# Optimization experiments

Measured on AMD Instinct MI355X. Metric: run time of the kernel, lower is better.

Reference implementation:

```python
import jax, jax.numpy as jnp
import numpy as np

B, E, S, DIM, HID, H = 8, 512, 1024, 1024, 1024, 8  # S == DIM == HID by construction


def setup_inputs() -> dict:
    key = jax.random.key(0)
    ks = jax.random.split(key, 7)
    x = jax.random.normal(ks[0], (B, E, S), dtype=jnp.float32)
    # per-head projection Linear(dim, hidden_dim): weight [H, hidden, dim], bias [H, hidden]
    proj_w = jax.random.normal(ks[1], (H, HID, DIM), dtype=jnp.float32) / np.sqrt(DIM)
    proj_b = jax.random.normal(ks[2], (H, HID), dtype=jnp.float32) * 0.02
    # per-head ColRepeatCausalLinear: weight [H, S] (torch.randn(1, dim)), bias [H, S] (zeros init)
    mix_w = jax.random.normal(ks[3], (H, S), dtype=jnp.float32)
    mix_b = jnp.zeros((H, S), dtype=jnp.float32)
    # out_proj Linear(dim, dim)
    out_w = jax.random.normal(ks[4], (DIM, DIM), dtype=jnp.float32) / np.sqrt(DIM)
    out_b = jax.random.normal(ks[5], (DIM,), dtype=jnp.float32) * 0.02
    return {"x": x, "proj_w": proj_w, "proj_b": proj_b, "mix_w": mix_w,
            "mix_b": mix_b, "out_w": out_w, "out_b": out_b, "index": 0}


def reference(x, proj_w, proj_b, mix_w, mix_b, out_w, out_b, index):
    # Per-head linear projection on the last axis (grouped GEMM across heads).
    # proj: [B, H, E, HID]
    proj = jnp.einsum('bes,hds->bhed', x, proj_w) + proj_b[None, :, None, :]
    # ColRepeatCausalLinear parallel path with decay_value == 1:
    # W[i, j] = v[j] for j >= i  =>  (x @ W)[..., j] = v[j] * cumsum(x, -1)[..., j]
    mixed = mix_w[None, :, None, :] * jnp.cumsum(proj, axis=-1) + mix_b[None, :, None, :]
    # torch.cat(activations, dim=1): [B, H*E, S]
    hidden = mixed.reshape(B, H * E, S)
    # out_proj Linear(dim, dim) on last axis
    out = hidden @ out_w.T + out_b
    return out
```

## Files before the change

kernel.cpp:

```cpp
#include <hip/hip_runtime.h>

#define NH    8
#define NE    512
#define NB    8
#define ND    1024
#define NROW  4096

typedef unsigned short u16;
typedef __attribute__((ext_vector_type(8))) short short8;
typedef __attribute__((ext_vector_type(4))) float f32x4;

__device__ __forceinline__ u16 f2bf(float f) {
  unsigned int u = __float_as_uint(f);
  u += 0x7fffu + ((u >> 16) & 1u);
  return (u16)(u >> 16);
}

__device__ __forceinline__ void gload16(const u16* g, u16* l) {
  __builtin_amdgcn_global_load_lds(
      (const __attribute__((address_space(1))) unsigned int*)(const void*)g,
      (__attribute__((address_space(3))) unsigned int*)(void*)l, 16, 0, 0);
}

__global__ __launch_bounds__(256) void fused_pre_kernel(
    const float* __restrict__ X, u16* __restrict__ Xb,
    const float* __restrict__ W, u16* __restrict__ Wt,
    const float* __restrict__ out_w, const float* __restrict__ mix_w,
    const float* __restrict__ mix_b, const float* __restrict__ proj_b,
    const float* __restrict__ out_b,
    u16* __restrict__ Afac, float* __restrict__ Kc) {
  __shared__ float tile[64][65];
  __shared__ float wsum[4];
  __shared__ float red[4];
  const int bz = blockIdx.x;
  const int t  = threadIdx.x;

  if (bz < 1024) {
    const int o = bz;
    const int lane = t & 63, wave = t >> 6;
    float ow[4];
#pragma unroll
    for (int k = 0; k < 4; ++k) ow[k] = out_w[(size_t)o * ND + 1023 - (4 * t + k)];
    float ob = out_b[o];
#pragma unroll 1
    for (int h = 0; h < NH; ++h) {
      const float* mwr = mix_w + (size_t)h * ND;
      const float* mbr = mix_b + (size_t)h * ND;
      const float* pbr = proj_b + (size_t)h * ND;
      float l[4];
      float run = 0.f, mbdot = 0.f;
#pragma unroll
      for (int k = 0; k < 4; ++k) {
        int j = 1023 - (4 * t + k);
        mbdot += ow[k] * mbr[j];
        run += ow[k] * mwr[j];
        l[k] = run;
      }
      float tsum = run;
      float sc = tsum;
#pragma unroll
      for (int d = 1; d < 64; d <<= 1) {
        float other = __shfl_up(sc, d);
        if (lane >= d) sc += other;
      }
      if (lane == 63) wsum[wave] = sc;
      __syncthreads();
      float wprefix = 0.f;
      for (int w = 0; w < wave; ++w) wprefix += wsum[w];
      float excl = wprefix + sc - tsum;

      float cdot = 0.f;
      ushort4 pack;
      u16* pk = (u16*)&pack;
#pragma unroll
      for (int k = 0; k < 4; ++k) {
        int d = 1023 - (4 * t + k);
        float a = excl + l[k];
        cdot += a * pbr[d];
        pk[3 - k] = f2bf(a);
      }
      *(ushort4*)(Afac + ((size_t)(h * ND + o)) * ND + (1020 - 4 * t)) = pack;

      float tot = cdot + mbdot;
#pragma unroll
      for (int m = 32; m >= 1; m >>= 1) tot += __shfl_xor(tot, m);
      if (lane == 0) red[wave] = tot;
      __syncthreads();
      if (t == 0) Kc[h * ND + o] = red[0] + red[1] + red[2] + red[3] + ob;
    }
  } else if (bz < 3072) {
    const int f  = bz - 1024;
    const int h  = f >> 8;
    const int d0 = ((f >> 4) & 15) * 64;
    const int s0 = (f & 15) * 64;
    const int tr = t >> 4;
    const int tc = t & 15;
#pragma unroll
    for (int i = 0; i < 4; ++i) {
      int d = tr + i * 16;
      float4 v = *(const float4*)(W + ((size_t)h * ND + d0 + d) * ND + s0 + tc * 4);
      tile[d][tc * 4 + 0] = v.x;
      tile[d][tc * 4 + 1] = v.y;
      tile[d][tc * 4 + 2] = v.z;
      tile[d][tc * 4 + 3] = v.w;
    }
    __syncthreads();
#pragma unroll
    for (int i = 0; i < 4; ++i) {
      int s  = tr + i * 16;
      int dd = tc * 4;
      ushort4 o;
      o.x = f2bf(tile[dd + 0][s]);
      o.y = f2bf(tile[dd + 1][s]);
      o.z = f2bf(tile[dd + 2][s]);
      o.w = f2bf(tile[dd + 3][s]);
      *(ushort4*)(Wt + ((size_t)h * ND + s0 + s) * ND + d0 + dd) = o;
    }
  } else {
    int i = (bz - 3072) * 256 + t;
    float4 v = ((const float4*)X)[i];
    ushort4 o;
    o.x = f2bf(v.x); o.y = f2bf(v.y); o.z = f2bf(v.z); o.w = f2bf(v.w);
    ((ushort4*)Xb)[i] = o;
  }
}

#define MFMA_(d, a, b) d = __builtin_amdgcn_mfma_f32_16x16x32_bf16(a, b, d, 0, 0, 0)
#define NOVM ((void)0)
#define VM6 asm volatile("s_waitcnt vmcnt(6)" ::: "memory")
#define VM5 asm volatile("s_waitcnt vmcnt(5)" ::: "memory")
#define VM0 asm volatile("s_waitcnt vmcnt(0)" ::: "memory")

#define PHASE(q, b, STAGE_STMT, VMSTMT) do {                                   \
    short8 a00 = ldA(b, 2*(q),     0);                                         \
    short8 a01 = ldA(b, 2*(q),     1);                                         \
    short8 a10 = ldA(b, 2*(q) + 1, 0);                                         \
    short8 a11 = ldA(b, 2*(q) + 1, 1);                                         \
    if ((q) == 0) {                                                            \
      bf00 = ldB(b, 0, 0); bf01 = ldB(b, 0, 1);                                \
      bf10 = ldB(b, 1, 0); bf11 = ldB(b, 1, 1);                                \
      bf20 = ldB(b, 2, 0); bf21 = ldB(b, 2, 1);                                \
      bf30 = ldB(b, 3, 0); bf31 = ldB(b, 3, 1);                                \
    }                                                                          \
    STAGE_STMT;                                                                \
    __builtin_amdgcn_sched_barrier(0);                                         \
    VMSTMT;                                                                    \
    __builtin_amdgcn_s_barrier();                                              \
    asm volatile("s_waitcnt lgkmcnt(0)" ::: "memory");                         \
    __builtin_amdgcn_sched_barrier(0);                                         \
    __builtin_amdgcn_s_setprio(1);                                             \
    MFMA_(acc[2*(q)  ][0], a00, bf00);                                         \
    MFMA_(acc[2*(q)  ][1], a00, bf10);                                         \
    MFMA_(acc[2*(q)  ][2], a00, bf20);                                         \
    MFMA_(acc[2*(q)  ][3], a00, bf30);                                         \
    MFMA_(acc[2*(q)+1][0], a10, bf00);                                         \
    MFMA_(acc[2*(q)+1][1], a10, bf10);                                         \
    MFMA_(acc[2*(q)+1][2], a10, bf20);                                         \
    MFMA_(acc[2*(q)+1][3], a10, bf30);                                         \
    MFMA_(acc[2*(q)  ][0], a01, bf01);                                         \
    MFMA_(acc[2*(q)  ][1], a01, bf11);                                         \
    MFMA_(acc[2*(q)  ][2], a01, bf21);                                         \
    MFMA_(acc[2*(q)  ][3], a01, bf31);                                         \
    MFMA_(acc[2*(q)+1][0], a11, bf01);                                         \
    MFMA_(acc[2*(q)+1][1], a11, bf11);                                         \
    MFMA_(acc[2*(q)+1][2], a11, bf21);                                         \
    MFMA_(acc[2*(q)+1][3], a11, bf31);                                         \
    __builtin_amdgcn_s_setprio(0);                                             \
    __builtin_amdgcn_s_barrier();                                              \
  } while (0)

#define PHASE1(q, b, STAGE_STMT, VMSTMT) do {                                  \
    short8 a0 = ldA(b, (q), 0);                                                \
    short8 a1 = ldA(b, (q), 1);                                                \
    if ((q) == 0) {                                                            \
      bf00 = ldB(b, 0, 0); bf01 = ldB(b, 0, 1);                                \
      bf10 = ldB(b, 1, 0); bf11 = ldB(b, 1, 1);                                \
      bf20 = ldB(b, 2, 0); bf21 = ldB(b, 2, 1);                                \
      bf30 = ldB(b, 3, 0); bf31 = ldB(b, 3, 1);                                \
    }                                                                          \
    STAGE_STMT;                                                                \
    __builtin_amdgcn_sched_barrier(0);                                         \
    VMSTMT;                                                                    \
    __builtin_amdgcn_s_barrier();                                              \
    asm volatile("s_waitcnt lgkmcnt(0)" ::: "memory");                         \
    __builtin_amdgcn_sched_barrier(0);                                         \
    __builtin_amdgcn_s_setprio(1);                                             \
    MFMA_(acc[(q)][0], a0, bf00);                                              \
    MFMA_(acc[(q)][1], a0, bf10);                                              \
    MFMA_(acc[(q)][2], a0, bf20);                                              \
    MFMA_(acc[(q)][3], a0, bf30);                                              \
    MFMA_(acc[(q)][0], a1, bf01);                                              \
    MFMA_(acc[(q)][1], a1, bf11);                                              \
    MFMA_(acc[(q)][2], a1, bf21);                                              \
    MFMA_(acc[(q)][3], a1, bf31);                                              \
    __builtin_amdgcn_s_setprio(0);                                             \
    __builtin_amdgcn_s_barrier();                                              \
  } while (0)

#define GEMM_8PH_BODY(ASRC, BSRC)                                              \
  const int tid  = threadIdx.x;                                                \
  const int lane = tid & 63;                                                   \
  const int wave = tid >> 6;                                                   \
  const int wm   = wave >> 2;                                                  \
  const int wn   = wave & 3;                                                   \
  const int li8 = lane >> 3;                                                   \
  const int lc  = (lane & 7) ^ li8;                                            \
  const size_t stSrc = (size_t)li8 * ND + lc * 8;                              \
  const int stDst = lane * 8;                                                  \
  const u16* aSrc = (ASRC) + stSrc;                                            \
  const u16* bSrc = (BSRC) + stSrc;                                            \
  const int fr  = lane & 15;                                                   \
  const int rg  = lane >> 4;                                                   \
  const int ca0 = (((lane >> 4)    ) ^ (lane & 7)) * 8;                        \
  const int ca1 = (((lane >> 4) + 4) ^ (lane & 7)) * 8;                        \
  const int aOff = (wm * 128 + fr) * 64;                                       \
  const int bOff = 16384 + (wn * 64 + fr) * 64;                                \
  auto stageA = [&](int h, int t, int b) {                                     \
    _Pragma("unroll")                                                          \
    for (int jj = 0; jj < 2; ++jj) {                                           \
      int j = 2 * wave + jj;                                                   \
      int R = ((j >> 3) << 7) + h * 64 + ((j & 7) << 3);                       \
      gload16(aSrc + (size_t)R * ND + t * 64, lds + b * 32768 + R * 64 + stDst); \
    }                                                                          \
  };                                                                           \
  auto stageB = [&](int h, int t, int b) {                                     \
    _Pragma("unroll")                                                          \
    for (int jj = 0; jj < 2; ++jj) {                                           \
      int j = 2 * wave + jj;                                                   \
      int R = h * 128 + j * 8;                                                 \
      gload16(bSrc + (size_t)R * ND + t * 64, lds + b * 32768 + 16384 + R * 64 + stDst); \
    }                                                                          \
  };                                                                           \
  auto ldA = [&](int b, int mi, int kk) -> short8 {                            \
    return *(const short8*)(lds + b * 32768 + aOff + mi * 1024 + (kk ? ca1 : ca0)); \
  };                                                                           \
  auto ldB = [&](int b, int ni, int kk) -> short8 {                            \
    return *(const short8*)(lds + b * 32768 + bOff + ni * 1024 + (kk ? ca1 : ca0)); \
  };                                                                           \
  f32x4 acc[8][4];                                                             \
  f32x4 z = {0.f, 0.f, 0.f, 0.f};                                              \
  _Pragma("unroll")                                                            \
  for (int i = 0; i < 8; ++i)                                                  \
    _Pragma("unroll")                                                          \
    for (int j = 0; j < 4; ++j) acc[i][j] = z;                                 \
  short8 bf00, bf01, bf10, bf11, bf20, bf21, bf30, bf31;                       \
  stageA(0, 0, 0); stageA(1, 0, 0);                                            \
  stageB(0, 0, 0); stageB(1, 0, 0);                                            \
  stageB(0, 1, 1); stageB(1, 1, 1);                                            \
  stageA(0, 1, 1);                                                             \
  asm volatile("s_waitcnt vmcnt(6)" ::: "memory");                             \
  __builtin_amdgcn_s_barrier();                                                \
  _Pragma("unroll 1")                                                          \
  for (int it = 0; it < 7; ++it) {                                             \
    const int T = 2 * it;                                                      \
    PHASE(0, 0, stageA(1, T + 1, 1), NOVM);                                    \
    PHASE(1, 0, stageB(0, T + 2, 0), NOVM);                                    \
    PHASE(2, 0, stageB(1, T + 2, 0), NOVM);                                    \
    PHASE(3, 0, stageA(0, T + 2, 0), VM6);                                     \
    PHASE(0, 1, stageA(1, T + 2, 0), NOVM);                                    \
    PHASE(1, 1, stageB(0, T + 3, 1), NOVM);                                    \
    PHASE(2, 1, stageB(1, T + 3, 1), NOVM);                                    \
    PHASE(3, 1, stageA(0, T + 3, 1), VM6);                                     \
  }                                                                            \
  PHASE(0, 0, stageA(1, 15, 1), NOVM);                                         \
  PHASE(1, 0, NOVM, NOVM);                                                     \
  PHASE(2, 0, NOVM, NOVM);                                                     \
  PHASE(3, 0, NOVM, VM0);                                                      \
  PHASE(0, 1, NOVM, NOVM);                                                     \
  PHASE(1, 1, NOVM, NOVM);                                                     \
  PHASE(2, 1, NOVM, NOVM);                                                     \
  PHASE(3, 1, NOVM, NOVM);

__global__ __launch_bounds__(512, 2) void gemm1_8ph(const u16* __restrict__ Afac,
                                                    const u16* __restrict__ Wt,
                                                    u16* __restrict__ Mmat) {
  __shared__ __align__(16) u16 lds[49152];
  const int h  = blockIdx.z;
  const int m0 = blockIdx.y * 128;
  const int n0 = blockIdx.x * 256;
  const int tid  = threadIdx.x;
  const int lane = tid & 63;
  const int wave = tid >> 6;
  const int wm   = wave >> 2;
  const int wn   = wave & 3;
  const int li8 = lane >> 3;
  const int lc  = (lane & 7) ^ li8;
  const size_t stSrc = (size_t)li8 * ND + lc * 8;
  const int stDst = lane * 8;
  const u16* aSrc = Afac + ((size_t)h * ND + m0) * ND + stSrc;
  const u16* bSrc = Wt + ((size_t)h * ND + n0) * ND + stSrc;
  const int fr  = lane & 15;
  const int rg  = lane >> 4;
  const int ca0 = (((lane >> 4)    ) ^ (lane & 7)) * 8;
  const int ca1 = (((lane >> 4) + 4) ^ (lane & 7)) * 8;
  const int aOff = (wm * 64 + fr) * 64;
  const int bOff = 8192 + (wn * 64 + fr) * 64;

  auto stageA = [&](int h2, int t, int b) {
    int R = (wave >> 2) * 64 + h2 * 32 + (wave & 3) * 8;
    gload16(aSrc + (size_t)R * ND + t * 64, lds + b * 24576 + R * 64 + stDst);
  };
  auto stageB = [&](int h2, int t, int b) {
#pragma unroll
    for (int jj = 0; jj < 2; ++jj) {
      int j = 2 * wave + jj;
      int R = h2 * 128 + j * 8;
      gload16(bSrc + (size_t)R * ND + t * 64, lds + b * 24576 + 8192 + R * 64 + stDst);
    }
  };
  auto ldA = [&](int b, int mi, int kk) -> short8 {
    return *(const short8*)(lds + b * 24576 + aOff + mi * 1024 + (kk ? ca1 : ca0));
  };
  auto ldB = [&](int b, int ni, int kk) -> short8 {
    return *(const short8*)(lds + b * 24576 + bOff + ni * 1024 + (kk ? ca1 : ca0));
  };

  f32x4 acc[4][4];
  f32x4 z = {0.f, 0.f, 0.f, 0.f};
#pragma unroll
  for (int i = 0; i < 4; ++i)
#pragma unroll
    for (int j = 0; j < 4; ++j) acc[i][j] = z;
  short8 bf00, bf01, bf10, bf11, bf20, bf21, bf30, bf31;

  stageA(0, 0, 0); stageA(1, 0, 0);
  stageB(0, 0, 0); stageB(1, 0, 0);
  stageB(0, 1, 1); stageB(1, 1, 1);
  stageA(0, 1, 1);
  VM5;
  __builtin_amdgcn_s_barrier();

#pragma unroll 1
  for (int it = 0; it < 7; ++it) {
    const int T = 2 * it;
    PHASE1(0, 0, stageA(1, T + 1, 1), NOVM);
    PHASE1(1, 0, stageB(0, T + 2, 0), NOVM);
    PHASE1(2, 0, stageB(1, T + 2, 0), NOVM);
    PHASE1(3, 0, stageA(0, T + 2, 0), VM5);
    PHASE1(0, 1, stageA(1, T + 2, 0), NOVM);
    PHASE1(1, 1, stageB(0, T + 3, 1), NOVM);
    PHASE1(2, 1, stageB(1, T + 3, 1), NOVM);
    PHASE1(3, 1, stageA(0, T + 3, 1), VM5);
  }
  PHASE1(0, 0, stageA(1, 15, 1), NOVM);
  PHASE1(1, 0, NOVM, NOVM);
  PHASE1(2, 0, NOVM, NOVM);
  PHASE1(3, 0, NOVM, VM0);
  PHASE1(0, 1, NOVM, NOVM);
  PHASE1(1, 1, NOVM, NOVM);
  PHASE1(2, 1, NOVM, NOVM);
  PHASE1(3, 1, NOVM, NOVM);

  u16* Mh = Mmat + (size_t)h * ND * ND;
  const int r0 = m0 + wm * 64 + rg * 4;
  const int c0 = n0 + wn * 64 + fr;
#pragma unroll
  for (int mi = 0; mi < 4; ++mi) {
#pragma unroll
    for (int r = 0; r < 4; ++r) {
      u16* orow = Mh + (size_t)(r0 + mi * 16 + r) * ND + c0;
#pragma unroll
      for (int ni = 0; ni < 4; ++ni)
        orow[ni * 16] = f2bf(acc[mi][ni][r]);
    }
  }
}

__global__ __launch_bounds__(512, 2) void gemm2_8ph(const u16* __restrict__ Xb,
                                                    const u16* __restrict__ Bm,
                                                    const float* __restrict__ Kc,
                                                    float* __restrict__ Out) {
  __shared__ __align__(16) u16 lds[65536];
  const int bid = blockIdx.x;
  const int xcd = bid & 7;
  const int loc = bid >> 3;
  const int m0  = (((xcd >> 2) << 3) + (loc >> 3)) * 256;
  const int n0  = (((xcd & 3) << 3) + (loc & 7)) * 256;
  GEMM_8PH_BODY(Xb + (size_t)m0 * ND, Bm + (size_t)n0 * ND)

  const int hH = n0 >> 10;
  const int r0 = m0 + wm * 128 + rg * 4;
  const int c0 = n0 + wn * 64 + fr;
  const int o0 = c0 & 1023;
  float bias[4];
#pragma unroll
  for (int ni = 0; ni < 4; ++ni) bias[ni] = Kc[c0 + ni * 16];
#pragma unroll
  for (int mi = 0; mi < 8; ++mi) {
#pragma unroll
    for (int r = 0; r < 4; ++r) {
      int rb = r0 + mi * 16 + r;
      float* orow = Out + ((size_t)(rb >> 9) * 4096 + hH * 512 + (rb & 511)) * 1024 + o0;
#pragma unroll
      for (int ni = 0; ni < 4; ++ni)
        orow[ni * 16] = acc[mi][ni][r] + bias[ni];
    }
  }
}

extern "C" void kernel_launch(void* const* d_in, const int* in_sizes, int n_in,
                              void* d_out, int out_size, void* d_ws, size_t ws_size,
                              hipStream_t stream) {
  (void)in_sizes; (void)n_in; (void)out_size; (void)ws_size;
  const float* x      = (const float*)d_in[0];
  const float* proj_w = (const float*)d_in[1];
  const float* proj_b = (const float*)d_in[2];
  const float* mix_w  = (const float*)d_in[3];
  const float* mix_b  = (const float*)d_in[4];
  const float* out_w  = (const float*)d_in[5];
  const float* out_b  = (const float*)d_in[6];
  float* Out = (float*)d_out;

  u16* Wt   = (u16*)d_out;
  u16* Afac = (u16*)d_out + (size_t)8 * 1024 * 1024;
  u16*   Xb   = (u16*)d_ws;
  u16*   Mmat = (u16*)((char*)d_ws + ((size_t)8 << 20));
  float* Kc   = (float*)((char*)d_ws + ((size_t)24 << 20));

  fused_pre_kernel<<<7168, 256, 0, stream>>>(x, Xb, proj_w, Wt,
                                             out_w, mix_w, mix_b, proj_b, out_b,
                                             Afac, Kc);
  gemm1_8ph<<<dim3(4, 8, NH), 512, 0, stream>>>(Afac, Wt, Mmat);
  gemm2_8ph<<<512, 512, 0, stream>>>(Xb, Mmat, Kc, Out);
}
```

Measured before the change: 114.6 us.

## Retile second GEMM to 256x128 blocks with triple-buffered K=32 stages

Replaces the 256x256-tile, 8-phase second GEMM with a 256x128-tile kernel that uses K=32 slices, a three-stage LDS ring buffer and a smaller LDS footprint. Launch bounds go from 2 to 4 blocks per CU and the grid doubles to 1024 blocks, which should raise occupancy and shorten tail effects. In exchange, each block reuses less data per tile, B traffic rises, and there are more barriers per unit of K work.

```diff
diff --git a/kernel.cpp b/kernel.cpp
--- a/kernel.cpp
+++ b/kernel.cpp
@@ -127,47 +127,10 @@
 
 #define MFMA_(d, a, b) d = __builtin_amdgcn_mfma_f32_16x16x32_bf16(a, b, d, 0, 0, 0)
 #define NOVM ((void)0)
-#define VM6 asm volatile("s_waitcnt vmcnt(6)" ::: "memory")
+#define NOST ((void)0)
 #define VM5 asm volatile("s_waitcnt vmcnt(5)" ::: "memory")
+#define VM3 asm volatile("s_waitcnt vmcnt(3)" ::: "memory")
 #define VM0 asm volatile("s_waitcnt vmcnt(0)" ::: "memory")
-
-#define PHASE(q, b, STAGE_STMT, VMSTMT) do {                                   \
-    short8 a00 = ldA(b, 2*(q),     0);                                         \
-    short8 a01 = ldA(b, 2*(q),     1);                                         \
-    short8 a10 = ldA(b, 2*(q) + 1, 0);                                         \
-    short8 a11 = ldA(b, 2*(q) + 1, 1);                                         \
-    if ((q) == 0) {                                                            \
-      bf00 = ldB(b, 0, 0); bf01 = ldB(b, 0, 1);                                \
-      bf10 = ldB(b, 1, 0); bf11 = ldB(b, 1, 1);                                \
-      bf20 = ldB(b, 2, 0); bf21 = ldB(b, 2, 1);                                \
-      bf30 = ldB(b, 3, 0); bf31 = ldB(b, 3, 1);                                \
-    }                                                                          \
-    STAGE_STMT;                                                                \
-    __builtin_amdgcn_sched_barrier(0);                                         \
-    VMSTMT;                                                                    \
-    __builtin_amdgcn_s_barrier();                                              \
-    asm volatile("s_waitcnt lgkmcnt(0)" ::: "memory");                         \
-    __builtin_amdgcn_sched_barrier(0);                                         \
-    __builtin_amdgcn_s_setprio(1);                                             \
-    MFMA_(acc[2*(q)  ][0], a00, bf00);                                         \
-    MFMA_(acc[2*(q)  ][1], a00, bf10);                                         \
-    MFMA_(acc[2*(q)  ][2], a00, bf20);                                         \
-    MFMA_(acc[2*(q)  ][3], a00, bf30);                                         \
-    MFMA_(acc[2*(q)+1][0], a10, bf00);                                         \
-    MFMA_(acc[2*(q)+1][1], a10, bf10);                                         \
-    MFMA_(acc[2*(q)+1][2], a10, bf20);                                         \
-    MFMA_(acc[2*(q)+1][3], a10, bf30);                                         \
-    MFMA_(acc[2*(q)  ][0], a01, bf01);                                         \
-    MFMA_(acc[2*(q)  ][1], a01, bf11);                                         \
-    MFMA_(acc[2*(q)  ][2], a01, bf21);                                         \
-    MFMA_(acc[2*(q)  ][3], a01, bf31);                                         \
-    MFMA_(acc[2*(q)+1][0], a11, bf01);                                         \
-    MFMA_(acc[2*(q)+1][1], a11, bf11);                                         \
-    MFMA_(acc[2*(q)+1][2], a11, bf21);                                         \
-    MFMA_(acc[2*(q)+1][3], a11, bf31);                                         \
-    __builtin_amdgcn_s_setprio(0);                                             \
-    __builtin_amdgcn_s_barrier();                                              \
-  } while (0)
 
 #define PHASE1(q, b, STAGE_STMT, VMSTMT) do {                                  \
     short8 a0 = ldA(b, (q), 0);                                                \
@@ -197,80 +160,6 @@
     __builtin_amdgcn_s_barrier();                                              \
   } while (0)
 
-#define GEMM_8PH_BODY(ASRC, BSRC)                                              \
-  const int tid  = threadIdx.x;                                                \
-  const int lane = tid & 63;                                                   \
-  const int wave = tid >> 6;                                                   \
-  const int wm   = wave >> 2;                                                  \
-  const int wn   = wave & 3;                                                   \
-  const int li8 = lane >> 3;                                                   \
-  const int lc  = (lane & 7) ^ li8;                                            \
-  const size_t stSrc = (size_t)li8 * ND + lc * 8;                              \
-  const int stDst = lane * 8;                                                  \
-  const u16* aSrc = (ASRC) + stSrc;                                            \
-  const u16* bSrc = (BSRC) + stSrc;                                            \
-  const int fr  = lane & 15;                                                   \
-  const int rg  = lane >> 4;                                                   \
-  const int ca0 = (((lane >> 4)    ) ^ (lane & 7)) * 8;                        \
-  const int ca1 = (((lane >> 4) + 4) ^ (lane & 7)) * 8;                        \
-  const int aOff = (wm * 128 + fr) * 64;                                       \
-  const int bOff = 16384 + (wn * 64 + fr) * 64;                                \
-  auto stageA = [&](int h, int t, int b) {                                     \
-    _Pragma("unroll")                                                          \
-    for (int jj = 0; jj < 2; ++jj) {                                           \
-      int j = 2 * wave + jj;                                                   \
-      int R = ((j >> 3) << 7) + h * 64 + ((j & 7) << 3);                       \
-      gload16(aSrc + (size_t)R * ND + t * 64, lds + b * 32768 + R * 64 + stDst); \
-    }                                                                          \
-  };                                                                           \
-  auto stageB = [&](int h, int t, int b) {                                     \
-    _Pragma("unroll")                                                          \
-    for (int jj = 0; jj < 2; ++jj) {                                           \
-      int j = 2 * wave + jj;                                                   \
-      int R = h * 128 + j * 8;                                                 \
-      gload16(bSrc + (size_t)R * ND + t * 64, lds + b * 32768 + 16384 + R * 64 + stDst); \
-    }                                                                          \
-  };                                                                           \
-  auto ldA = [&](int b, int mi, int kk) -> short8 {                            \
-    return *(const short8*)(lds + b * 32768 + aOff + mi * 1024 + (kk ? ca1 : ca0)); \
-  };                                                                           \
-  auto ldB = [&](int b, int ni, int kk) -> short8 {                            \
-    return *(const short8*)(lds + b * 32768 + bOff + ni * 1024 + (kk ? ca1 : ca0)); \
-  };                                                                           \
-  f32x4 acc[8][4];                                                             \
-  f32x4 z = {0.f, 0.f, 0.f, 0.f};                                              \
-  _Pragma("unroll")                                                            \
-  for (int i = 0; i < 8; ++i)                                                  \
-    _Pragma("unroll")                                                          \
-    for (int j = 0; j < 4; ++j) acc[i][j] = z;                                 \
-  short8 bf00, bf01, bf10, bf11, bf20, bf21, bf30, bf31;                       \
-  stageA(0, 0, 0); stageA(1, 0, 0);                                            \
-  stageB(0, 0, 0); stageB(1, 0, 0);                                            \
-  stageB(0, 1, 1); stageB(1, 1, 1);                                            \
-  stageA(0, 1, 1);                                                             \
-  asm volatile("s_waitcnt vmcnt(6)" ::: "memory");                             \
-  __builtin_amdgcn_s_barrier();                                                \
-  _Pragma("unroll 1")                                                          \
-  for (int it = 0; it < 7; ++it) {                                             \
-    const int T = 2 * it;                                                      \
-    PHASE(0, 0, stageA(1, T + 1, 1), NOVM);                                    \
-    PHASE(1, 0, stageB(0, T + 2, 0), NOVM);                                    \
-    PHASE(2, 0, stageB(1, T + 2, 0), NOVM);                                    \
-    PHASE(3, 0, stageA(0, T + 2, 0), VM6);                                     \
-    PHASE(0, 1, stageA(1, T + 2, 0), NOVM);                                    \
-    PHASE(1, 1, stageB(0, T + 3, 1), NOVM);                                    \
-    PHASE(2, 1, stageB(1, T + 3, 1), NOVM);                                    \
-    PHASE(3, 1, stageA(0, T + 3, 1), VM6);                                     \
-  }                                                                            \
-  PHASE(0, 0, stageA(1, 15, 1), NOVM);                                         \
-  PHASE(1, 0, NOVM, NOVM);                                                     \
-  PHASE(2, 0, NOVM, NOVM);                                                     \
-  PHASE(3, 0, NOVM, VM0);                                                      \
-  PHASE(0, 1, NOVM, NOVM);                                                     \
-  PHASE(1, 1, NOVM, NOVM);                                                     \
-  PHASE(2, 1, NOVM, NOVM);                                                     \
-  PHASE(3, 1, NOVM, NOVM);
-
 __global__ __launch_bounds__(512, 2) void gemm1_8ph(const u16* __restrict__ Afac,
                                                     const u16* __restrict__ Wt,
                                                     u16* __restrict__ Mmat) {
@@ -366,27 +255,112 @@
   }
 }
 
-__global__ __launch_bounds__(512, 2) void gemm2_8ph(const u16* __restrict__ Xb,
-                                                    const u16* __restrict__ Bm,
-                                                    const float* __restrict__ Kc,
-                                                    float* __restrict__ Out) {
-  __shared__ __align__(16) u16 lds[65536];
+#define PHASEB(BR, STAGE_STMT, VMSTMT) do {                                    \
+    short8 a0 = ldA2(BR, 0);                                                   \
+    short8 a1 = ldA2(BR, 1);                                                   \
+    short8 a2 = ldA2(BR, 2);                                                   \
+    short8 a3 = ldA2(BR, 3);                                                   \
+    short8 b0 = ldB2(BR, 0);                                                   \
+    short8 b1 = ldB2(BR, 1);                                                   \
+    short8 b2 = ldB2(BR, 2);                                                   \
+    short8 b3 = ldB2(BR, 3);                                                   \
+    STAGE_STMT;                                                                \
+    __builtin_amdgcn_sched_barrier(0);                                         \
+    VMSTMT;                                                                    \
+    __builtin_amdgcn_s_barrier();                                              \
+    asm volatile("s_waitcnt lgkmcnt(0)" ::: "memory");                         \
+    __builtin_amdgcn_sched_barrier(0);                                         \
+    __builtin_amdgcn_s_setprio(1);                                             \
+    MFMA_(acc[0][0], a0, b0); MFMA_(acc[0][1], a0, b1);                        \
+    MFMA_(acc[0][2], a0, b2); MFMA_(acc[0][3], a0, b3);                        \
+    MFMA_(acc[1][0], a1, b0); MFMA_(acc[1][1], a1, b1);                        \
+    MFMA_(acc[1][2], a1, b2); MFMA_(acc[1][3], a1, b3);                        \
+    MFMA_(acc[2][0], a2, b0); MFMA_(acc[2][1], a2, b1);                        \
+    MFMA_(acc[2][2], a2, b2); MFMA_(acc[2][3], a2, b3);                        \
+    MFMA_(acc[3][0], a3, b0); MFMA_(acc[3][1], a3, b1);                        \
+    MFMA_(acc[3][2], a3, b2); MFMA_(acc[3][3], a3, b3);                        \
+    __builtin_amdgcn_s_setprio(0);                                             \
+    __builtin_amdgcn_s_barrier();                                              \
+  } while (0)
+
+#define STG2(kof, bOff) do {                                                   \
+    gload16(aS0 + (kof), lds + (bOff) + aD0);                                  \
+    gload16(aS1 + (kof), lds + (bOff) + aD1);                                  \
+    gload16(bS0 + (kof), lds + (bOff) + 8192 + bD0);                           \
+  } while (0)
+
+__global__ __launch_bounds__(512, 4) void gemm2b(const u16* __restrict__ Xb,
+                                                 const u16* __restrict__ Bm,
+                                                 const float* __restrict__ Kc,
+                                                 float* __restrict__ Out) {
+  __shared__ __align__(16) u16 lds[36864];
+  const int tid  = threadIdx.x;
+  const int lane = tid & 63;
+  const int wave = tid >> 6;
+  const int wm   = wave >> 1;
+  const int wn   = wave & 1;
+
   const int bid = blockIdx.x;
   const int xcd = bid & 7;
   const int loc = bid >> 3;
-  const int m0  = (((xcd >> 2) << 3) + (loc >> 3)) * 256;
-  const int n0  = (((xcd & 3) << 3) + (loc & 7)) * 256;
-  GEMM_8PH_BODY(Xb + (size_t)m0 * ND, Bm + (size_t)n0 * ND)
+  const int m0  = ((xcd & 1) * 8 + (loc >> 4)) * 256;
+  const int n0  = ((xcd >> 1) * 16 + (loc & 15)) * 128;
+
+  const int lcS = (lane & 3) ^ ((lane >> 3) & 3);
+  const size_t stSrc = (size_t)(lane >> 2) * ND + lcS * 8;
+  const int stDst = lane * 8;
+
+  const u16* aS0 = Xb + ((size_t)(m0 + wave * 32)) * ND + stSrc;
+  const u16* aS1 = Xb + ((size_t)(m0 + wave * 32 + 16)) * ND + stSrc;
+  const u16* bS0 = Bm + ((size_t)(n0 + wave * 16)) * ND + stSrc;
+  const int aD0 = (wave * 32) * 32 + stDst;
+  const int aD1 = (wave * 32 + 16) * 32 + stDst;
+  const int bD0 = (wave * 16) * 32 + stDst;
+
+  const int fr  = lane & 15;
+  const int rg  = lane >> 4;
+  const int caA = ((lane >> 4) ^ ((lane >> 1) & 3)) * 8;
+  const int aBase = (wm * 64 + fr) * 32 + caA;
+  const int bBase = 8192 + (wn * 64 + fr) * 32 + caA;
+
+  auto ldA2 = [&](int bR, int mi) -> short8 {
+    return *(const short8*)(lds + bR + aBase + mi * 512);
+  };
+  auto ldB2 = [&](int bR, int ni) -> short8 {
+    return *(const short8*)(lds + bR + bBase + ni * 512);
+  };
+
+  f32x4 acc[4][4];
+  f32x4 z = {0.f, 0.f, 0.f, 0.f};
+#pragma unroll
+  for (int i = 0; i < 4; ++i)
+#pragma unroll
+    for (int j = 0; j < 4; ++j) acc[i][j] = z;
+
+  STG2(0, 0);
+  STG2(32, 12288);
+  VM3;
+  __builtin_amdgcn_s_barrier();
+
+#pragma unroll 1
+  for (int it = 0; it < 10; ++it) {
+    const int T = 3 * it;
+    PHASEB(0,     STG2((T + 2) * 32, 24576), VM3);
+    PHASEB(12288, STG2((T + 3) * 32, 0),     VM3);
+    PHASEB(24576, STG2((T + 4) * 32, 12288), VM3);
+  }
+  PHASEB(0,     NOST, VM0);
+  PHASEB(12288, NOST, NOVM);
 
   const int hH = n0 >> 10;
-  const int r0 = m0 + wm * 128 + rg * 4;
+  const int r0 = m0 + wm * 64 + rg * 4;
   const int c0 = n0 + wn * 64 + fr;
   const int o0 = c0 & 1023;
   float bias[4];
 #pragma unroll
-  for (int ni = 0; ni < 4; ++ni) bias[ni] = Kc[c0 + ni * 16];
-#pragma unroll
-  for (int mi = 0; mi < 8; ++mi) {
+  for (int ni = 0; ni < 4; ++ni) bias[ni] = Kc[hH * 1024 + o0 + ni * 16];
+#pragma unroll
+  for (int mi = 0; mi < 4; ++mi) {
 #pragma unroll
     for (int r = 0; r < 4; ++r) {
       int rb = r0 + mi * 16 + r;
@@ -421,5 +395,5 @@
                                              out_w, mix_w, mix_b, proj_b, out_b,
                                              Afac, Kc);
   gemm1_8ph<<<dim3(4, 8, NH), 512, 0, stream>>>(Afac, Wt, Mmat);
-  gemm2_8ph<<<512, 512, 0, stream>>>(Xb, Mmat, Kc, Out);
-}
+  gemm2b<<<1024, 512, 0, stream>>>(Xb, Mmat, Kc, Out);
+}
```

After: 121.5 us. 6.0% more time.
